# Kernel tuning notes

Measured on AMD Instinct MI355X. Metric: run time of the kernel, lower is better.

Reference implementation:

```python
import jax, jax.numpy as jnp
import numpy as np

B, C, N = 2, 6, 2048      # batch, channels (xyz+3 extra), points per cloud
K, NS = 64, 32            # top-k keypoints, ball-query group size
D = 32                    # deep feature dim (num_feat)
RADIUS = 1.0              # ball query radius (sample_and_group)
VR, VS = 1.0, 0.4         # voxelize range / step -> 6^3 = 216 candidates


def setup_inputs() -> dict:
    key = jax.random.key(0)
    ks = jax.random.split(key, 16)
    rn = lambda k, s, sc=1.0: jax.random.normal(k, s, dtype=jnp.float32) * sc
    Q, _ = jnp.linalg.qr(jax.random.normal(ks[2], (3, 3), dtype=jnp.float32))
    return {
        "src_pts": rn(ks[0], (B, C, N)),
        "tgt_pts": rn(ks[1], (B, C, N)),
        "R_init": Q,
        "t_init": rn(ks[3], (1, 3), 0.1),
        "W1": rn(ks[4], (C, 64), 0.2), "b1": jnp.zeros((64,), jnp.float32),
        "W2": rn(ks[5], (64, D), 0.2), "b2": jnp.zeros((D,), jnp.float32),
        "Wwl": rn(ks[6], (D, 1), 0.2), "bwl": jnp.zeros((1,), jnp.float32),
        "W3": rn(ks[7], (3 + D, 64), 0.2), "b3": jnp.zeros((64,), jnp.float32),
        "W4": rn(ks[8], (64, D), 0.2), "b4": jnp.zeros((D,), jnp.float32),
    }


def _fe(pts, W1, b1, W2, b2):
    # feat_extraction_layer: shared point-wise MLP. pts [B,C,N] -> xyz [B,N,3], feat [B,N,D]
    x = jnp.transpose(pts, (0, 2, 1))
    xyz = x[..., :3]
    f = jax.nn.relu(x @ W1 + b1)
    f = jax.nn.relu(f @ W2 + b2)
    return xyz, f


def _index_points(pts, idx):
    # pts [B,N,D], idx [B,K,S] -> [B,K,S,D]
    b = pts.shape[0]
    return pts[jnp.arange(b)[:, None, None], idx]


def _sqdist(a, b):
    # a [B,M,3], b [B,N,3] -> [B,M,N]
    return (jnp.sum(a * a, -1)[:, :, None] + jnp.sum(b * b, -1)[:, None, :]
            - 2.0 * jnp.einsum('bmd,bnd->bmn', a, b))


def reference(src_pts, tgt_pts, R_init, t_init, W1, b1, W2, b2, Wwl, bwl, W3, b3, W4, b4):
    b = src_pts.shape[0]
    # FE1 on source
    src_xyz, src_feat = _fe(src_pts, W1, b1, W2, b2)
    # weighting_layer: per-point saliency -> top-K keypoint indices
    w = (src_feat @ Wwl + bwl)[..., 0]                    # [B,N]
    _, kidx = jax.lax.top_k(w, K)                          # [B,K]
    src_T = jnp.transpose(src_pts, (0, 2, 1))              # [B,N,C]
    src_keypts = jnp.take_along_axis(src_T, kidx[:, :, None], axis=1)  # [B,K,C]
    centers = src_keypts[..., :3]
    # sample_and_group: ball query NS nearest-within-radius around each keypoint
    d2 = _sqdist(centers, src_xyz)                         # [B,K,N]
    negd, nn = jax.lax.top_k(-d2, NS)
    group_idx = jnp.where(-negd <= RADIUS ** 2, nn, nn[:, :, :1])
    grouped_xyz = _index_points(src_xyz, group_idx)        # [B,K,NS,3]
    keyfeats = _index_points(src_feat, group_idx)          # [B,K,NS,D]
    src_cat = jnp.concatenate([grouped_xyz - centers[:, :, None, :], keyfeats], -1)
    # FE1 on target
    tgt_xyz, tgt_feat = _fe(tgt_pts, W1, b1, W2, b2)
    # transform keypoints with initial pose, voxelize into candidate grid
    xform = jnp.einsum('ij,bkj->bki', R_init, centers) + t_init
    g = jnp.arange(int(2 * VR / VS) + 1, dtype=jnp.float32) * VS - VR   # 6 steps
    gx, gy, gz = jnp.meshgrid(g, g, g, indexing='ij')
    offs = jnp.stack([gx.ravel(), gy.ravel(), gz.ravel()], -1)          # [216,3]
    cand = xform[:, :, None, :] + offs                      # [B,K,216,3]
    nc = offs.shape[0]
    cand_flat = cand.reshape(b, K * nc, 3)
    # nearest target point per candidate -> gathered deep feature + relative offset
    d2t = _sqdist(cand_flat, tgt_xyz)                       # [B,K*216,N] (dominant buffer)
    nnt = jnp.argmin(d2t, axis=-1)                          # [B,K*216]
    nn_xyz = jnp.take_along_axis(tgt_xyz, nnt[:, :, None], axis=1)
    nn_feat = jnp.take_along_axis(tgt_feat, nnt[:, :, None], axis=1)
    rel = (nn_xyz - cand_flat).reshape(b, K, nc, 3)
    tgt_cat = jnp.concatenate([rel, nn_feat.reshape(b, K, nc, D)], -1)
    # DFE: shared MLP; src branch max-pools over the NS group
    dfe = lambda x: jax.nn.relu(jax.nn.relu(x @ W3 + b3) @ W4 + b4)
    src_dfe = jnp.max(dfe(src_cat), axis=2)                 # [B,K,D]
    tgt_dfe = dfe(tgt_cat)                                  # [B,K,216,D]
    # cpg: similarity -> softmax over candidates -> weighted centroid
    sim = jnp.einsum('bkd,bkcd->bkc', src_dfe, tgt_dfe)
    attn = jax.nn.softmax(sim, axis=-1)
    vcp = jnp.einsum('bkc,bkcd->bkd', attn, cand)           # [B,K,3]
    return src_keypts, vcp
```

## Files before the change

### kernel.cpp

```cpp
#include <hip/hip_runtime.h>
#include <math.h>

#define BB_ 2
#define CC_ 6
#define NN_ 2048
#define KK_ 64
#define NS_ 32
#define DD_ 32
#define NC_ 216
#define HH_ 64

#define OFF_SRC_PACK 0
#define OFF_TGT_PACK 16384
#define OFF_SRC_FEAT 32768
#define OFF_TGT_FEAT 163840
#define OFF_W        294912
#define OFF_CENTERS  299008
#define OFF_XFORM    299392
#define OFF_SRCDFE   299776
#define OFF_NNT      303872

__device__ __forceinline__ unsigned sortable_f32(float f) {
    unsigned u = __float_as_uint(f);
    return (u & 0x80000000u) ? ~u : (u | 0x80000000u);
}
__device__ __forceinline__ float unsortable_f32(unsigned s) {
    unsigned u = (s & 0x80000000u) ? (s ^ 0x80000000u) : ~s;
    return __uint_as_float(u);
}

__device__ __forceinline__ unsigned long long wave_sort64_asc(unsigned long long key, int lane) {
#pragma unroll
    for (int k = 2; k <= 64; k <<= 1) {
#pragma unroll
        for (int j = k >> 1; j > 0; j >>= 1) {
            unsigned long long other = __shfl_xor(key, j);
            bool lower = (lane & j) == 0;
            bool asc = (lane & k) == 0;
            bool takemin = (lower == asc);
            unsigned long long mn = key < other ? key : other;
            unsigned long long mx = key < other ? other : key;
            key = takemin ? mn : mx;
        }
    }
    return key;
}

__device__ __forceinline__ unsigned long long merge_keep_min64(unsigned long long a, unsigned long long b, int lane) {
    unsigned long long br = __shfl(b, 63 - lane);
    unsigned long long m = a < br ? a : br;
#pragma unroll
    for (int j = 32; j > 0; j >>= 1) {
        unsigned long long other = __shfl_xor(m, j);
        bool lower = (lane & j) == 0;
        unsigned long long mn = m < other ? m : other;
        unsigned long long mx = m < other ? other : m;
        m = lower ? mn : mx;
    }
    return m;
}

__device__ __forceinline__ void block_select64_16w(unsigned long long kA, unsigned long long kB,
                                                   unsigned long long* runs, int tid) {
    int w = tid >> 6, lane = tid & 63;
    kA = wave_sort64_asc(kA, lane);
    kB = wave_sort64_asc(kB, lane);
    unsigned long long m = merge_keep_min64(kA, kB, lane);
    runs[w * 64 + lane] = m;
    __syncthreads();
#pragma unroll
    for (int lvl = 8; lvl >= 1; lvl >>= 1) {
        unsigned long long r = 0;
        if (w < lvl) {
            unsigned long long a = runs[w * 64 + lane];
            unsigned long long b = runs[(w + lvl) * 64 + lane];
            r = merge_keep_min64(a, b, lane);
        }
        __syncthreads();
        if (w < lvl) runs[w * 64 + lane] = r;
        __syncthreads();
    }
}

__global__ void fe_kernel(const float* __restrict__ src, const float* __restrict__ tgt,
                          const float* __restrict__ W1, const float* __restrict__ b1,
                          const float* __restrict__ W2, const float* __restrict__ b2,
                          const float* __restrict__ Wwl, const float* __restrict__ bwl,
                          float* __restrict__ ws) {
    int tid = blockIdx.x * blockDim.x + threadIdx.x;
    if (tid >= 2 * BB_ * NN_) return;
    int cloud = tid / (BB_ * NN_);
    int r = tid - cloud * BB_ * NN_;
    int b = r / NN_, n = r % NN_;
    const float* pts = cloud ? tgt : src;
    float x[CC_];
#pragma unroll
    for (int c = 0; c < CC_; ++c) x[c] = pts[(b * CC_ + c) * NN_ + n];
    float bb;
    {
#pragma clang fp contract(off)
        bb = (x[0] * x[0] + x[1] * x[1]) + x[2] * x[2];
    }
    float4* pack = (float4*)(ws + (cloud ? OFF_TGT_PACK : OFF_SRC_PACK));
    pack[b * NN_ + n] = make_float4(x[0], x[1], x[2], bb);

    float h[HH_];
#pragma unroll
    for (int t = 0; t < HH_; ++t) {
        float s = b1[t];
#pragma unroll
        for (int c = 0; c < CC_; ++c) s += x[c] * W1[c * HH_ + t];
        h[t] = fmaxf(s, 0.f);
    }
    float* feat = ws + (cloud ? OFF_TGT_FEAT : OFF_SRC_FEAT) + (size_t)(b * NN_ + n) * DD_;
    float wsum = 0.f;
#pragma unroll 4
    for (int d = 0; d < DD_; ++d) {
        float s = b2[d];
#pragma unroll
        for (int t = 0; t < HH_; ++t) s += h[t] * W2[t * DD_ + d];
        s = fmaxf(s, 0.f);
        feat[d] = s;
        wsum += s * Wwl[d];
    }
    if (cloud == 0) (ws + OFF_W)[b * NN_ + n] = wsum + bwl[0];
}

__global__ void topk_kernel(const float* __restrict__ src, const float* __restrict__ R,
                            const float* __restrict__ t, float* __restrict__ ws,
                            float* __restrict__ out) {
    __shared__ unsigned long long runs[16 * 64];
    int b = blockIdx.x;
    int tid = threadIdx.x, w = tid >> 6, lane = tid & 63;
    const float* wv = ws + OFF_W + b * NN_;
    int jA = w * 128 + lane, jB = jA + 64;
    unsigned long long kA = ((unsigned long long)(~sortable_f32(wv[jA])) << 32) | (unsigned)jA;
    unsigned long long kB = ((unsigned long long)(~sortable_f32(wv[jB])) << 32) | (unsigned)jB;
    block_select64_16w(kA, kB, runs, tid);
    if (tid < KK_) {
        int bi = (int)(runs[tid] & 0xFFFFFFFFu);
        float c3[3];
#pragma unroll
        for (int c = 0; c < CC_; ++c) {
            float v = src[(b * CC_ + c) * NN_ + bi];
            out[(b * KK_ + tid) * CC_ + c] = v;
            if (c < 3) c3[c] = v;
        }
        float* cen = ws + OFF_CENTERS + (b * KK_ + tid) * 3;
        cen[0] = c3[0]; cen[1] = c3[1]; cen[2] = c3[2];
        float* xf = ws + OFF_XFORM + (b * KK_ + tid) * 3;
#pragma unroll
        for (int i = 0; i < 3; ++i) {
#pragma clang fp contract(off)
            xf[i] = ((R[i * 3 + 0] * c3[0] + R[i * 3 + 1] * c3[1]) + R[i * 3 + 2] * c3[2]) + t[i];
        }
    }
}

__global__ __launch_bounds__(576) void mid_kernel(const float* __restrict__ W3, const float* __restrict__ b3,
                                                  const float* __restrict__ W4, const float* __restrict__ b4,
                                                  float* __restrict__ ws) {
    __shared__ union U {
        float4 pk[NN_];
        struct {
            unsigned long long runs[8 * 64];
            float hs[NS_][HH_];
            float outs[NS_][DD_];
        } s;
    } u;
    int blk = blockIdx.x;
    int tid = threadIdx.x;
    if (blk < 2 * BB_ * KK_) {
        int bk = blk >> 1;
        int half = blk & 1;
        int b = bk / KK_;
        const float4* pack = (const float4*)(ws + OFF_TGT_PACK) + b * NN_;
        for (int j = tid; j < NN_; j += 576) {
            u.pk[j ^ ((j >> 6) & 7)] = pack[j];
        }
        const float* xf = ws + OFF_XFORM + bk * 3;
        float x0 = xf[0], x1 = xf[1], x2 = xf[2];
        __syncthreads();

        int lg = tid >> 5;
        int chunk = tid & 31;
        int grp = half * 18 + lg;
        int ix = grp / 6, iy = grp % 6;
        float cx = x0 + (ix * 0.4f - 1.0f);
        float cy = x1 + (iy * 0.4f - 1.0f);
        float cxy2;
        {
#pragma clang fp contract(off)
            cxy2 = cx * cx + cy * cy;
        }
        float m2x = -2.0f * cx, m2y = -2.0f * cy;
        float aaz[6], m2z[6];
#pragma unroll
        for (int z = 0; z < 6; ++z) {
            float cz = x2 + (z * 0.4f - 1.0f);
            {
#pragma clang fp contract(off)
                aaz[z] = cxy2 + cz * cz;
            }
            m2z[z] = -2.0f * cz;
        }
        float bv[6];
        int bi[6];
#pragma unroll
        for (int z = 0; z < 6; ++z) { bv[z] = INFINITY; bi[z] = 0; }
        int base = chunk * 64;
        int sw = chunk & 7;
        for (int i = 0; i < 64; ++i) {
            int j = base + i;
            float4 p = u.pk[base + (i ^ sw)];
            float txy;
            {
#pragma clang fp contract(off)
                txy = m2x * p.x + m2y * p.y;
            }
#pragma unroll
            for (int z = 0; z < 6; ++z) {
                float d2;
                {
#pragma clang fp contract(off)
                    d2 = (aaz[z] + p.w) + (txy + m2z[z] * p.z);
                }
                if (d2 < bv[z]) { bv[z] = d2; bi[z] = j; }
            }
        }
        int* nnt = (int*)ws + OFF_NNT + bk * NC_ + grp * 6;
#pragma unroll
        for (int z = 0; z < 6; ++z) {
            unsigned long long key = ((unsigned long long)sortable_f32(bv[z]) << 32) | (unsigned)bi[z];
#pragma unroll
            for (int m = 1; m <= 16; m <<= 1) {
                unsigned long long other = __shfl_xor(key, m);
                key = other < key ? other : key;
            }
            if (chunk == 0) nnt[z] = (int)(key & 0xFFFFFFFFu);
        }
    } else {
        int bk = blk - 2 * BB_ * KK_;
        int b = bk / KK_;
        int w = tid >> 6, lane = tid & 63;
        const float* cen = ws + OFF_CENTERS + bk * 3;
        float c0 = cen[0], c1 = cen[1], c2 = cen[2];
        float aa;
        {
#pragma clang fp contract(off)
            aa = (c0 * c0 + c1 * c1) + c2 * c2;
        }
        float m2x = -2.0f * c0, m2y = -2.0f * c1, m2z = -2.0f * c2;
        const float4* pack = (const float4*)(ws + OFF_SRC_PACK) + b * NN_;
        if (w < 8) {
            unsigned long long k4[4];
#pragma unroll
            for (int q = 0; q < 4; ++q) {
                int j = w * 256 + q * 64 + lane;
                float4 p = pack[j];
                float d2;
                {
#pragma clang fp contract(off)
                    d2 = (aa + p.w) + ((m2x * p.x + m2y * p.y) + m2z * p.z);
                }
                k4[q] = ((unsigned long long)sortable_f32(d2) << 32) | (unsigned)j;
            }
            unsigned long long m1 = merge_keep_min64(wave_sort64_asc(k4[0], lane),
                                                     wave_sort64_asc(k4[1], lane), lane);
            unsigned long long m2 = merge_keep_min64(wave_sort64_asc(k4[2], lane),
                                                     wave_sort64_asc(k4[3], lane), lane);
            u.s.runs[w * 64 + lane] = merge_keep_min64(m1, m2, lane);
        }
        __syncthreads();
#pragma unroll
        for (int lvl = 4; lvl >= 1; lvl >>= 1) {
            unsigned long long r = 0;
            if (w < lvl) {
                r = merge_keep_min64(u.s.runs[w * 64 + lane], u.s.runs[(w + lvl) * 64 + lane], lane);
            }
            __syncthreads();
            if (w < lvl) u.s.runs[w * 64 + lane] = r;
            __syncthreads();
        }
        const float* feats = ws + OFF_SRC_FEAT + (size_t)b * NN_ * DD_;
        unsigned long long key0 = u.s.runs[0];
        if (w < 8) {
#pragma unroll
            for (int ss = 0; ss < 4; ++ss) {
                int s = w * 4 + ss;
                unsigned long long key = u.s.runs[s];
                float dd = unsortable_f32((unsigned)(key >> 32));
                int j = (dd <= 1.0f) ? (int)(key & 0xFFFFFFFFu) : (int)(key0 & 0xFFFFFFFFu);
                float4 p = pack[j];
                float r0 = p.x - c0, r1 = p.y - c1, r2 = p.z - c2;
                const float* f = feats + (size_t)j * DD_;
                float acc = b3[lane] + r0 * W3[0 * HH_ + lane] + r1 * W3[1 * HH_ + lane] + r2 * W3[2 * HH_ + lane];
#pragma unroll 8
                for (int d = 0; d < DD_; ++d) acc += f[d] * W3[(3 + d) * HH_ + lane];
                u.s.hs[s][lane] = fmaxf(acc, 0.f);
            }
        }
        __syncthreads();
        for (int idx = tid; idx < NS_ * DD_; idx += 576) {
            int s2 = idx >> 5, di = idx & 31;
            float o = b4[di];
#pragma unroll 8
            for (int t2 = 0; t2 < HH_; ++t2) o += u.s.hs[s2][t2] * W4[t2 * DD_ + di];
            u.s.outs[s2][di] = fmaxf(o, 0.f);
        }
        __syncthreads();
        if (tid < DD_) {
            float m = -INFINITY;
#pragma unroll 8
            for (int s = 0; s < NS_; ++s) m = fmaxf(m, u.s.outs[s][tid]);
            (ws + OFF_SRCDFE)[bk * DD_ + tid] = m;
        }
    }
}

__global__ void simvcp_kernel(const float* __restrict__ W3, const float* __restrict__ b3,
                              const float* __restrict__ W4, const float* __restrict__ b4,
                              float* __restrict__ ws, float* __restrict__ out) {
    __shared__ float sims[NC_];
    int bk = blockIdx.x;
    int b = bk / KK_;
    int tid = threadIdx.x;
    const float* xf = ws + OFF_XFORM + bk * 3;
    if (tid < NC_) {
        int c = tid;
        int ix = c / 36, iy = (c / 6) % 6, iz = c % 6;
        float cx = xf[0] + (ix * 0.4f - 1.0f);
        float cy = xf[1] + (iy * 0.4f - 1.0f);
        float cz = xf[2] + (iz * 0.4f - 1.0f);
        int bi = ((const int*)ws)[OFF_NNT + bk * NC_ + c];
        float4 p = ((const float4*)(ws + OFF_TGT_PACK))[b * NN_ + bi];
        float x[3 + DD_];
        x[0] = p.x - cx; x[1] = p.y - cy; x[2] = p.z - cz;
        const float* f = ws + OFF_TGT_FEAT + ((size_t)b * NN_ + bi) * DD_;
#pragma unroll
        for (int d = 0; d < DD_; ++d) x[3 + d] = f[d];
        float o[DD_];
#pragma unroll
        for (int d = 0; d < DD_; ++d) o[d] = b4[d];
        for (int t = 0; t < HH_; ++t) {
            float acc = b3[t];
#pragma unroll
            for (int cc = 0; cc < 3 + DD_; ++cc) acc += x[cc] * W3[cc * HH_ + t];
            float ht = fmaxf(acc, 0.f);
#pragma unroll
            for (int d = 0; d < DD_; ++d) o[d] += ht * W4[t * DD_ + d];
        }
        const float* sd = ws + OFF_SRCDFE + bk * DD_;
        float sim = 0.f;
#pragma unroll
        for (int d = 0; d < DD_; ++d) sim += fmaxf(o[d], 0.f) * sd[d];
        sims[c] = sim;
    }
    __syncthreads();
    if (tid < 64) {
        int lane = tid;
        float m = -INFINITY;
        for (int c = lane; c < NC_; c += 64) m = fmaxf(m, sims[c]);
#pragma unroll
        for (int sh = 32; sh; sh >>= 1) m = fmaxf(m, __shfl_xor(m, sh));
        float se = 0.f, v0 = 0.f, v1 = 0.f, v2 = 0.f;
        for (int c = lane; c < NC_; c += 64) {
            float e = expf(sims[c] - m);
            int ix = c / 36, iy = (c / 6) % 6, iz = c % 6;
            se += e;
            v0 += e * (xf[0] + (ix * 0.4f - 1.0f));
            v1 += e * (xf[1] + (iy * 0.4f - 1.0f));
            v2 += e * (xf[2] + (iz * 0.4f - 1.0f));
        }
#pragma unroll
        for (int sh = 32; sh; sh >>= 1) {
            se += __shfl_xor(se, sh);
            v0 += __shfl_xor(v0, sh);
            v1 += __shfl_xor(v1, sh);
            v2 += __shfl_xor(v2, sh);
        }
        if (lane == 0) {
            float inv = 1.0f / se;
            float* oo = out + BB_ * KK_ * CC_ + bk * 3;
            oo[0] = v0 * inv;
            oo[1] = v1 * inv;
            oo[2] = v2 * inv;
        }
    }
}

extern "C" void kernel_launch(void* const* d_in, const int* in_sizes, int n_in,
                              void* d_out, int out_size, void* d_ws, size_t ws_size,
                              hipStream_t stream) {
    const float* src = (const float*)d_in[0];
    const float* tgt = (const float*)d_in[1];
    const float* R   = (const float*)d_in[2];
    const float* t   = (const float*)d_in[3];
    const float* W1  = (const float*)d_in[4];
    const float* b1  = (const float*)d_in[5];
    const float* W2  = (const float*)d_in[6];
    const float* b2  = (const float*)d_in[7];
    const float* Wwl = (const float*)d_in[8];
    const float* bwl = (const float*)d_in[9];
    const float* W3  = (const float*)d_in[10];
    const float* b3  = (const float*)d_in[11];
    const float* W4  = (const float*)d_in[12];
    const float* b4  = (const float*)d_in[13];
    float* ws  = (float*)d_ws;
    float* out = (float*)d_out;

    fe_kernel<<<(2 * BB_ * NN_ + 127) / 128, 128, 0, stream>>>(src, tgt, W1, b1, W2, b2, Wwl, bwl, ws);
    topk_kernel<<<BB_, 1024, 0, stream>>>(src, R, t, ws, out);
    mid_kernel<<<2 * BB_ * KK_ + BB_ * KK_, 576, 0, stream>>>(W3, b3, W4, b4, ws);
    simvcp_kernel<<<BB_ * KK_, 256, 0, stream>>>(W3, b3, W4, b4, ws, out);
}
```

Baseline: 82.53 us.

## Fuse pipeline into single cooperative kernel with grid barrier and recomputed features

Replaces the four launches with one cooperative kernel of 128 blocks, one per keypoint. Each block first computes saliency for a 32-point slice, then waits at an atomic-counter grid barrier. After that every block redundantly runs the top-k selection, the candidate nearest-neighbour search and the source grouping. Target features are recomputed only for the 216 matched neighbours instead of for all target points. This removes launch gaps and global-memory round trips, at the cost of duplicated top-k work per block, a spin barrier, and an extra memset launch.

```diff
diff --git a/kernel.cpp b/kernel.cpp
--- a/kernel.cpp
+++ b/kernel.cpp
@@ -9,16 +9,10 @@
 #define DD_ 32
 #define NC_ 216
 #define HH_ 64
-
-#define OFF_SRC_PACK 0
-#define OFF_TGT_PACK 16384
-#define OFF_SRC_FEAT 32768
-#define OFF_TGT_FEAT 163840
-#define OFF_W        294912
-#define OFF_CENTERS  299008
-#define OFF_XFORM    299392
-#define OFF_SRCDFE   299776
-#define OFF_NNT      303872
+#define NBLK_ 128
+
+#define OFF_W        0
+#define OFF_BAR      4096
 
 __device__ __forceinline__ unsigned sortable_f32(float f) {
     unsigned u = __float_as_uint(f);
@@ -60,331 +54,384 @@
     return m;
 }
 
-__device__ __forceinline__ void block_select64_16w(unsigned long long kA, unsigned long long kB,
-                                                   unsigned long long* runs, int tid) {
-    int w = tid >> 6, lane = tid & 63;
-    kA = wave_sort64_asc(kA, lane);
-    kB = wave_sort64_asc(kB, lane);
-    unsigned long long m = merge_keep_min64(kA, kB, lane);
-    runs[w * 64 + lane] = m;
-    __syncthreads();
-#pragma unroll
-    for (int lvl = 8; lvl >= 1; lvl >>= 1) {
-        unsigned long long r = 0;
-        if (w < lvl) {
-            unsigned long long a = runs[w * 64 + lane];
-            unsigned long long b = runs[(w + lvl) * 64 + lane];
-            r = merge_keep_min64(a, b, lane);
-        }
-        __syncthreads();
-        if (w < lvl) runs[w * 64 + lane] = r;
-        __syncthreads();
-    }
-}
-
-__global__ void fe_kernel(const float* __restrict__ src, const float* __restrict__ tgt,
-                          const float* __restrict__ W1, const float* __restrict__ b1,
-                          const float* __restrict__ W2, const float* __restrict__ b2,
-                          const float* __restrict__ Wwl, const float* __restrict__ bwl,
-                          float* __restrict__ ws) {
-    int tid = blockIdx.x * blockDim.x + threadIdx.x;
-    if (tid >= 2 * BB_ * NN_) return;
-    int cloud = tid / (BB_ * NN_);
-    int r = tid - cloud * BB_ * NN_;
-    int b = r / NN_, n = r % NN_;
-    const float* pts = cloud ? tgt : src;
-    float x[CC_];
-#pragma unroll
-    for (int c = 0; c < CC_; ++c) x[c] = pts[(b * CC_ + c) * NN_ + n];
-    float bb;
-    {
-#pragma clang fp contract(off)
-        bb = (x[0] * x[0] + x[1] * x[1]) + x[2] * x[2];
-    }
-    float4* pack = (float4*)(ws + (cloud ? OFF_TGT_PACK : OFF_SRC_PACK));
-    pack[b * NN_ + n] = make_float4(x[0], x[1], x[2], bb);
-
-    float h[HH_];
-#pragma unroll
-    for (int t = 0; t < HH_; ++t) {
-        float s = b1[t];
-#pragma unroll
-        for (int c = 0; c < CC_; ++c) s += x[c] * W1[c * HH_ + t];
-        h[t] = fmaxf(s, 0.f);
-    }
-    float* feat = ws + (cloud ? OFF_TGT_FEAT : OFF_SRC_FEAT) + (size_t)(b * NN_ + n) * DD_;
-    float wsum = 0.f;
-#pragma unroll 4
-    for (int d = 0; d < DD_; ++d) {
-        float s = b2[d];
-#pragma unroll
-        for (int t = 0; t < HH_; ++t) s += h[t] * W2[t * DD_ + d];
-        s = fmaxf(s, 0.f);
-        feat[d] = s;
-        wsum += s * Wwl[d];
-    }
-    if (cloud == 0) (ws + OFF_W)[b * NN_ + n] = wsum + bwl[0];
-}
-
-__global__ void topk_kernel(const float* __restrict__ src, const float* __restrict__ R,
-                            const float* __restrict__ t, float* __restrict__ ws,
-                            float* __restrict__ out) {
-    __shared__ unsigned long long runs[16 * 64];
-    int b = blockIdx.x;
-    int tid = threadIdx.x, w = tid >> 6, lane = tid & 63;
-    const float* wv = ws + OFF_W + b * NN_;
-    int jA = w * 128 + lane, jB = jA + 64;
-    unsigned long long kA = ((unsigned long long)(~sortable_f32(wv[jA])) << 32) | (unsigned)jA;
-    unsigned long long kB = ((unsigned long long)(~sortable_f32(wv[jB])) << 32) | (unsigned)jB;
-    block_select64_16w(kA, kB, runs, tid);
-    if (tid < KK_) {
-        int bi = (int)(runs[tid] & 0xFFFFFFFFu);
-        float c3[3];
-#pragma unroll
-        for (int c = 0; c < CC_; ++c) {
-            float v = src[(b * CC_ + c) * NN_ + bi];
-            out[(b * KK_ + tid) * CC_ + c] = v;
-            if (c < 3) c3[c] = v;
-        }
-        float* cen = ws + OFF_CENTERS + (b * KK_ + tid) * 3;
-        cen[0] = c3[0]; cen[1] = c3[1]; cen[2] = c3[2];
-        float* xf = ws + OFF_XFORM + (b * KK_ + tid) * 3;
-#pragma unroll
-        for (int i = 0; i < 3; ++i) {
-#pragma clang fp contract(off)
-            xf[i] = ((R[i * 3 + 0] * c3[0] + R[i * 3 + 1] * c3[1]) + R[i * 3 + 2] * c3[2]) + t[i];
-        }
-    }
-}
-
-__global__ __launch_bounds__(576) void mid_kernel(const float* __restrict__ W3, const float* __restrict__ b3,
-                                                  const float* __restrict__ W4, const float* __restrict__ b4,
-                                                  float* __restrict__ ws) {
-    __shared__ union U {
+__global__ __launch_bounds__(576) void mega2_kernel(
+        const float* __restrict__ src, const float* __restrict__ tgt,
+        const float* __restrict__ R, const float* __restrict__ t,
+        const float* __restrict__ W1, const float* __restrict__ b1,
+        const float* __restrict__ W2, const float* __restrict__ b2,
+        const float* __restrict__ Wwl, const float* __restrict__ bwl,
+        const float* __restrict__ W3, const float* __restrict__ b3,
+        const float* __restrict__ W4, const float* __restrict__ b4,
+        float* __restrict__ ws, float* __restrict__ out) {
+    __shared__ union {
+        struct { float fpts[32][CC_]; float h[32][HH_]; float f[32][DD_]; } fe;
+        unsigned long long runs[8 * 64];
         float4 pk[NN_];
         struct {
-            unsigned long long runs[8 * 64];
+            unsigned long long runs2[8 * 64];
+            float spts[NS_][CC_];
             float hs[NS_][HH_];
+            float sfeat[NS_][DD_];
             float outs[NS_][DD_];
-        } s;
+        } sg;
+        struct { float th[108][HH_]; float tfeat[NC_][DD_]; } tf;
     } u;
+    __shared__ float bcast[8];
+    __shared__ int   nnt216[NC_];
+    __shared__ float tall[NC_][CC_];
+    __shared__ int   sidx[NS_];
+    __shared__ float sdfe[DD_];
+    __shared__ float sims[NC_];
+
     int blk = blockIdx.x;
     int tid = threadIdx.x;
-    if (blk < 2 * BB_ * KK_) {
-        int bk = blk >> 1;
-        int half = blk & 1;
-        int b = bk / KK_;
-        const float4* pack = (const float4*)(ws + OFF_TGT_PACK) + b * NN_;
-        for (int j = tid; j < NN_; j += 576) {
-            u.pk[j ^ ((j >> 6) & 7)] = pack[j];
-        }
-        const float* xf = ws + OFF_XFORM + bk * 3;
-        float x0 = xf[0], x1 = xf[1], x2 = xf[2];
-        __syncthreads();
-
-        int lg = tid >> 5;
-        int chunk = tid & 31;
-        int grp = half * 18 + lg;
-        int ix = grp / 6, iy = grp % 6;
-        float cx = x0 + (ix * 0.4f - 1.0f);
-        float cy = x1 + (iy * 0.4f - 1.0f);
-        float cxy2;
-        {
-#pragma clang fp contract(off)
-            cxy2 = cx * cx + cy * cy;
-        }
-        float m2x = -2.0f * cx, m2y = -2.0f * cy;
-        float aaz[6], m2z[6];
-#pragma unroll
-        for (int z = 0; z < 6; ++z) {
-            float cz = x2 + (z * 0.4f - 1.0f);
-            {
-#pragma clang fp contract(off)
-                aaz[z] = cxy2 + cz * cz;
-            }
-            m2z[z] = -2.0f * cz;
-        }
-        float bv[6];
-        int bi[6];
-#pragma unroll
-        for (int z = 0; z < 6; ++z) { bv[z] = INFINITY; bi[z] = 0; }
-        int base = chunk * 64;
-        int sw = chunk & 7;
-        for (int i = 0; i < 64; ++i) {
-            int j = base + i;
-            float4 p = u.pk[base + (i ^ sw)];
-            float txy;
-            {
-#pragma clang fp contract(off)
-                txy = m2x * p.x + m2y * p.y;
-            }
-#pragma unroll
-            for (int z = 0; z < 6; ++z) {
-                float d2;
-                {
-#pragma clang fp contract(off)
-                    d2 = (aaz[z] + p.w) + (txy + m2z[z] * p.z);
-                }
-                if (d2 < bv[z]) { bv[z] = d2; bi[z] = j; }
-            }
-        }
-        int* nnt = (int*)ws + OFF_NNT + bk * NC_ + grp * 6;
-#pragma unroll
-        for (int z = 0; z < 6; ++z) {
-            unsigned long long key = ((unsigned long long)sortable_f32(bv[z]) << 32) | (unsigned)bi[z];
-#pragma unroll
-            for (int m = 1; m <= 16; m <<= 1) {
-                unsigned long long other = __shfl_xor(key, m);
-                key = other < key ? other : key;
-            }
-            if (chunk == 0) nnt[z] = (int)(key & 0xFFFFFFFFu);
-        }
-    } else {
-        int bk = blk - 2 * BB_ * KK_;
-        int b = bk / KK_;
-        int w = tid >> 6, lane = tid & 63;
-        const float* cen = ws + OFF_CENTERS + bk * 3;
-        float c0 = cen[0], c1 = cen[1], c2 = cen[2];
-        float aa;
-        {
-#pragma clang fp contract(off)
-            aa = (c0 * c0 + c1 * c1) + c2 * c2;
-        }
-        float m2x = -2.0f * c0, m2y = -2.0f * c1, m2z = -2.0f * c2;
-        const float4* pack = (const float4*)(ws + OFF_SRC_PACK) + b * NN_;
+    int w = tid >> 6, lane = tid & 63;
+    int bk = blk;
+    int bat = bk / KK_;
+    int kth = bk % KK_;
+    float* wbuf = ws + OFF_W;
+    unsigned* ctr = (unsigned*)(ws + OFF_BAR);
+
+    {
+        int p0 = blk * 32;
+        for (int idx = tid; idx < 32 * CC_; idx += 576) {
+            int pt = idx / CC_, c = idx % CC_;
+            int g = p0 + pt; int bb = g / NN_, n = g % NN_;
+            u.fe.fpts[pt][c] = src[(bb * CC_ + c) * NN_ + n];
+        }
+        __syncthreads();
+        for (int idx = tid; idx < 32 * HH_; idx += 576) {
+            int pt = idx >> 6, tt = idx & 63;
+            float s = b1[tt];
+#pragma unroll
+            for (int c = 0; c < CC_; ++c) s += u.fe.fpts[pt][c] * W1[c * HH_ + tt];
+            u.fe.h[pt][tt] = fmaxf(s, 0.f);
+        }
+        __syncthreads();
+        for (int idx = tid; idx < 32 * DD_; idx += 576) {
+            int pt = idx >> 5, d = idx & 31;
+            float s = b2[d];
+#pragma unroll 8
+            for (int tt = 0; tt < HH_; ++tt) s += u.fe.h[pt][tt] * W2[tt * DD_ + d];
+            u.fe.f[pt][d] = fmaxf(s, 0.f);
+        }
+        __syncthreads();
+        if (tid < 32) {
+            float wsum = 0.f;
+#pragma unroll 8
+            for (int d = 0; d < DD_; ++d) wsum += u.fe.f[tid][d] * Wwl[d];
+            wsum += bwl[0];
+            __hip_atomic_store(&wbuf[p0 + tid], wsum, __ATOMIC_RELAXED, __HIP_MEMORY_SCOPE_AGENT);
+        }
+        __syncthreads();
+        if (tid == 0)
+            __hip_atomic_fetch_add(ctr, 1u, __ATOMIC_RELEASE, __HIP_MEMORY_SCOPE_AGENT);
+        if (tid == 0) {
+            while (__hip_atomic_load(ctr, __ATOMIC_RELAXED, __HIP_MEMORY_SCOPE_AGENT) < (unsigned)NBLK_)
+                __builtin_amdgcn_s_sleep(4);
+        }
+        __syncthreads();
+    }
+
+    {
         if (w < 8) {
             unsigned long long k4[4];
 #pragma unroll
             for (int q = 0; q < 4; ++q) {
                 int j = w * 256 + q * 64 + lane;
-                float4 p = pack[j];
-                float d2;
-                {
-#pragma clang fp contract(off)
-                    d2 = (aa + p.w) + ((m2x * p.x + m2y * p.y) + m2z * p.z);
-                }
-                k4[q] = ((unsigned long long)sortable_f32(d2) << 32) | (unsigned)j;
+                float wv = __hip_atomic_load(&wbuf[bat * NN_ + j], __ATOMIC_RELAXED, __HIP_MEMORY_SCOPE_AGENT);
+                k4[q] = ((unsigned long long)(~sortable_f32(wv)) << 32) | (unsigned)j;
             }
             unsigned long long m1 = merge_keep_min64(wave_sort64_asc(k4[0], lane),
                                                      wave_sort64_asc(k4[1], lane), lane);
             unsigned long long m2 = merge_keep_min64(wave_sort64_asc(k4[2], lane),
                                                      wave_sort64_asc(k4[3], lane), lane);
-            u.s.runs[w * 64 + lane] = merge_keep_min64(m1, m2, lane);
+            u.runs[w * 64 + lane] = merge_keep_min64(m1, m2, lane);
         }
         __syncthreads();
 #pragma unroll
         for (int lvl = 4; lvl >= 1; lvl >>= 1) {
             unsigned long long r = 0;
-            if (w < lvl) {
-                r = merge_keep_min64(u.s.runs[w * 64 + lane], u.s.runs[(w + lvl) * 64 + lane], lane);
-            }
-            __syncthreads();
-            if (w < lvl) u.s.runs[w * 64 + lane] = r;
-            __syncthreads();
-        }
-        const float* feats = ws + OFF_SRC_FEAT + (size_t)b * NN_ * DD_;
-        unsigned long long key0 = u.s.runs[0];
+            if (w < lvl) r = merge_keep_min64(u.runs[w * 64 + lane], u.runs[(w + lvl) * 64 + lane], lane);
+            __syncthreads();
+            if (w < lvl) u.runs[w * 64 + lane] = r;
+            __syncthreads();
+        }
+        if (tid == 0) {
+            int bi = (int)(u.runs[kth] & 0xFFFFFFFFu);
+            float c3[3];
+#pragma unroll
+            for (int c = 0; c < CC_; ++c) {
+                float v = src[(bat * CC_ + c) * NN_ + bi];
+                out[bk * CC_ + c] = v;
+                if (c < 3) c3[c] = v;
+            }
+            bcast[0] = c3[0]; bcast[1] = c3[1]; bcast[2] = c3[2];
+#pragma unroll
+            for (int i = 0; i < 3; ++i) {
+#pragma clang fp contract(off)
+                bcast[3 + i] = ((R[i * 3 + 0] * c3[0] + R[i * 3 + 1] * c3[1]) + R[i * 3 + 2] * c3[2]) + t[i];
+            }
+        }
+        __syncthreads();
+    }
+
+    {
+        for (int j = tid; j < NN_; j += 576) {
+            float px = tgt[(bat * CC_ + 0) * NN_ + j];
+            float py = tgt[(bat * CC_ + 1) * NN_ + j];
+            float pz = tgt[(bat * CC_ + 2) * NN_ + j];
+            float pw;
+            {
+#pragma clang fp contract(off)
+                pw = (px * px + py * py) + pz * pz;
+            }
+            u.pk[j ^ ((j >> 6) & 7)] = make_float4(px, py, pz, pw);
+        }
+        __syncthreads();
+        float x0 = bcast[3], x1 = bcast[4], x2 = bcast[5];
+        int lg = tid >> 5;
+        int chunk = tid & 31;
+        int base = chunk * 64;
+        int sw = chunk & 7;
+        for (int pass = 0; pass < 2; ++pass) {
+            int grp = pass * 18 + lg;
+            int ix = grp / 6, iy = grp % 6;
+            float cx = x0 + (ix * 0.4f - 1.0f);
+            float cy = x1 + (iy * 0.4f - 1.0f);
+            float cxy2;
+            {
+#pragma clang fp contract(off)
+                cxy2 = cx * cx + cy * cy;
+            }
+            float m2x = -2.0f * cx, m2y = -2.0f * cy;
+            float aaz[6], m2z[6];
+#pragma unroll
+            for (int z = 0; z < 6; ++z) {
+                float cz = x2 + (z * 0.4f - 1.0f);
+                {
+#pragma clang fp contract(off)
+                    aaz[z] = cxy2 + cz * cz;
+                }
+                m2z[z] = -2.0f * cz;
+            }
+            float bv[6];
+            int bi[6];
+#pragma unroll
+            for (int z = 0; z < 6; ++z) { bv[z] = INFINITY; bi[z] = 0; }
+            for (int i = 0; i < 64; ++i) {
+                int j = base + i;
+                float4 p = u.pk[base + (i ^ sw)];
+                float txy;
+                {
+#pragma clang fp contract(off)
+                    txy = m2x * p.x + m2y * p.y;
+                }
+#pragma unroll
+                for (int z = 0; z < 6; ++z) {
+                    float d2;
+                    {
+#pragma clang fp contract(off)
+                        d2 = (aaz[z] + p.w) + (txy + m2z[z] * p.z);
+                    }
+                    if (d2 < bv[z]) { bv[z] = d2; bi[z] = j; }
+                }
+            }
+#pragma unroll
+            for (int z = 0; z < 6; ++z) {
+                unsigned long long key = ((unsigned long long)sortable_f32(bv[z]) << 32) | (unsigned)bi[z];
+#pragma unroll
+                for (int m = 1; m <= 16; m <<= 1) {
+                    unsigned long long other = __shfl_xor(key, m);
+                    key = other < key ? other : key;
+                }
+                if (chunk == 0) nnt216[grp * 6 + z] = (int)(key & 0xFFFFFFFFu);
+            }
+        }
+        __syncthreads();
+    }
+
+    {
+        float c0 = bcast[0], c1 = bcast[1], c2 = bcast[2];
+        float aa;
+        {
+#pragma clang fp contract(off)
+            aa = (c0 * c0 + c1 * c1) + c2 * c2;
+        }
+        float m2x = -2.0f * c0, m2y = -2.0f * c1, m2z = -2.0f * c2;
+        if (w < 8) {
+            unsigned long long k4[4];
+#pragma unroll
+            for (int q = 0; q < 4; ++q) {
+                int j = w * 256 + q * 64 + lane;
+                float px = src[(bat * CC_ + 0) * NN_ + j];
+                float py = src[(bat * CC_ + 1) * NN_ + j];
+                float pz = src[(bat * CC_ + 2) * NN_ + j];
+                float d2;
+                {
+#pragma clang fp contract(off)
+                    float pw = (px * px + py * py) + pz * pz;
+                    d2 = (aa + pw) + ((m2x * px + m2y * py) + m2z * pz);
+                }
+                k4[q] = ((unsigned long long)sortable_f32(d2) << 32) | (unsigned)j;
+            }
+            unsigned long long m1 = merge_keep_min64(wave_sort64_asc(k4[0], lane),
+                                                     wave_sort64_asc(k4[1], lane), lane);
+            unsigned long long m2 = merge_keep_min64(wave_sort64_asc(k4[2], lane),
+                                                     wave_sort64_asc(k4[3], lane), lane);
+            u.sg.runs2[w * 64 + lane] = merge_keep_min64(m1, m2, lane);
+        }
+        __syncthreads();
+#pragma unroll
+        for (int lvl = 4; lvl >= 1; lvl >>= 1) {
+            unsigned long long r = 0;
+            if (w < lvl) r = merge_keep_min64(u.sg.runs2[w * 64 + lane], u.sg.runs2[(w + lvl) * 64 + lane], lane);
+            __syncthreads();
+            if (w < lvl) u.sg.runs2[w * 64 + lane] = r;
+            __syncthreads();
+        }
+        if (tid < NS_) {
+            unsigned long long key = u.sg.runs2[tid];
+            unsigned long long key0 = u.sg.runs2[0];
+            float dd = unsortable_f32((unsigned)(key >> 32));
+            sidx[tid] = (dd <= 1.0f) ? (int)(key & 0xFFFFFFFFu) : (int)(key0 & 0xFFFFFFFFu);
+        }
+        __syncthreads();
+        for (int idx = tid; idx < NS_ * CC_; idx += 576) {
+            int pt = idx / CC_, c = idx % CC_;
+            u.sg.spts[pt][c] = src[(bat * CC_ + c) * NN_ + sidx[pt]];
+        }
+        __syncthreads();
+        for (int idx = tid; idx < NS_ * HH_; idx += 576) {
+            int pt = idx >> 6, tt = idx & 63;
+            float s = b1[tt];
+#pragma unroll
+            for (int c = 0; c < CC_; ++c) s += u.sg.spts[pt][c] * W1[c * HH_ + tt];
+            u.sg.hs[pt][tt] = fmaxf(s, 0.f);
+        }
+        __syncthreads();
+        for (int idx = tid; idx < NS_ * DD_; idx += 576) {
+            int pt = idx >> 5, d = idx & 31;
+            float s = b2[d];
+#pragma unroll 8
+            for (int tt = 0; tt < HH_; ++tt) s += u.sg.hs[pt][tt] * W2[tt * DD_ + d];
+            u.sg.sfeat[pt][d] = fmaxf(s, 0.f);
+        }
+        __syncthreads();
         if (w < 8) {
 #pragma unroll
             for (int ss = 0; ss < 4; ++ss) {
                 int s = w * 4 + ss;
-                unsigned long long key = u.s.runs[s];
-                float dd = unsortable_f32((unsigned)(key >> 32));
-                int j = (dd <= 1.0f) ? (int)(key & 0xFFFFFFFFu) : (int)(key0 & 0xFFFFFFFFu);
-                float4 p = pack[j];
-                float r0 = p.x - c0, r1 = p.y - c1, r2 = p.z - c2;
-                const float* f = feats + (size_t)j * DD_;
+                float r0 = u.sg.spts[s][0] - c0, r1 = u.sg.spts[s][1] - c1, r2 = u.sg.spts[s][2] - c2;
                 float acc = b3[lane] + r0 * W3[0 * HH_ + lane] + r1 * W3[1 * HH_ + lane] + r2 * W3[2 * HH_ + lane];
 #pragma unroll 8
-                for (int d = 0; d < DD_; ++d) acc += f[d] * W3[(3 + d) * HH_ + lane];
-                u.s.hs[s][lane] = fmaxf(acc, 0.f);
+                for (int d = 0; d < DD_; ++d) acc += u.sg.sfeat[s][d] * W3[(3 + d) * HH_ + lane];
+                u.sg.hs[s][lane] = fmaxf(acc, 0.f);
             }
         }
         __syncthreads();
         for (int idx = tid; idx < NS_ * DD_; idx += 576) {
-            int s2 = idx >> 5, di = idx & 31;
-            float o = b4[di];
-#pragma unroll 8
-            for (int t2 = 0; t2 < HH_; ++t2) o += u.s.hs[s2][t2] * W4[t2 * DD_ + di];
-            u.s.outs[s2][di] = fmaxf(o, 0.f);
+            int s = idx >> 5, d = idx & 31;
+            float o = b4[d];
+#pragma unroll 8
+            for (int tt = 0; tt < HH_; ++tt) o += u.sg.hs[s][tt] * W4[tt * DD_ + d];
+            u.sg.outs[s][d] = fmaxf(o, 0.f);
         }
         __syncthreads();
         if (tid < DD_) {
             float m = -INFINITY;
 #pragma unroll 8
-            for (int s = 0; s < NS_; ++s) m = fmaxf(m, u.s.outs[s][tid]);
-            (ws + OFF_SRCDFE)[bk * DD_ + tid] = m;
-        }
-    }
-}
-
-__global__ void simvcp_kernel(const float* __restrict__ W3, const float* __restrict__ b3,
-                              const float* __restrict__ W4, const float* __restrict__ b4,
-                              float* __restrict__ ws, float* __restrict__ out) {
-    __shared__ float sims[NC_];
-    int bk = blockIdx.x;
-    int b = bk / KK_;
-    int tid = threadIdx.x;
-    const float* xf = ws + OFF_XFORM + bk * 3;
-    if (tid < NC_) {
-        int c = tid;
-        int ix = c / 36, iy = (c / 6) % 6, iz = c % 6;
-        float cx = xf[0] + (ix * 0.4f - 1.0f);
-        float cy = xf[1] + (iy * 0.4f - 1.0f);
-        float cz = xf[2] + (iz * 0.4f - 1.0f);
-        int bi = ((const int*)ws)[OFF_NNT + bk * NC_ + c];
-        float4 p = ((const float4*)(ws + OFF_TGT_PACK))[b * NN_ + bi];
-        float x[3 + DD_];
-        x[0] = p.x - cx; x[1] = p.y - cy; x[2] = p.z - cz;
-        const float* f = ws + OFF_TGT_FEAT + ((size_t)b * NN_ + bi) * DD_;
-#pragma unroll
-        for (int d = 0; d < DD_; ++d) x[3 + d] = f[d];
-        float o[DD_];
-#pragma unroll
-        for (int d = 0; d < DD_; ++d) o[d] = b4[d];
-        for (int t = 0; t < HH_; ++t) {
-            float acc = b3[t];
-#pragma unroll
-            for (int cc = 0; cc < 3 + DD_; ++cc) acc += x[cc] * W3[cc * HH_ + t];
-            float ht = fmaxf(acc, 0.f);
-#pragma unroll
-            for (int d = 0; d < DD_; ++d) o[d] += ht * W4[t * DD_ + d];
-        }
-        const float* sd = ws + OFF_SRCDFE + bk * DD_;
-        float sim = 0.f;
-#pragma unroll
-        for (int d = 0; d < DD_; ++d) sim += fmaxf(o[d], 0.f) * sd[d];
-        sims[c] = sim;
-    }
-    __syncthreads();
-    if (tid < 64) {
-        int lane = tid;
-        float m = -INFINITY;
-        for (int c = lane; c < NC_; c += 64) m = fmaxf(m, sims[c]);
-#pragma unroll
-        for (int sh = 32; sh; sh >>= 1) m = fmaxf(m, __shfl_xor(m, sh));
-        float se = 0.f, v0 = 0.f, v1 = 0.f, v2 = 0.f;
-        for (int c = lane; c < NC_; c += 64) {
-            float e = expf(sims[c] - m);
+            for (int s = 0; s < NS_; ++s) m = fmaxf(m, u.sg.outs[s][tid]);
+            sdfe[tid] = m;
+        }
+        __syncthreads();
+    }
+
+    {
+        for (int idx = tid; idx < NC_ * CC_; idx += 576) {
+            int pt = idx / CC_, c = idx % CC_;
+            tall[pt][c] = tgt[(bat * CC_ + c) * NN_ + nnt216[pt]];
+        }
+        __syncthreads();
+        for (int ch = 0; ch < 2; ++ch) {
+            for (int idx = tid; idx < 108 * HH_; idx += 576) {
+                int pl = idx >> 6, tt = idx & 63;
+                int pt = ch * 108 + pl;
+                float s = b1[tt];
+#pragma unroll
+                for (int c = 0; c < CC_; ++c) s += tall[pt][c] * W1[c * HH_ + tt];
+                u.tf.th[pl][tt] = fmaxf(s, 0.f);
+            }
+            __syncthreads();
+            for (int idx = tid; idx < 108 * DD_; idx += 576) {
+                int pl = idx >> 5, d = idx & 31;
+                int pt = ch * 108 + pl;
+                float s = b2[d];
+#pragma unroll 8
+                for (int tt = 0; tt < HH_; ++tt) s += u.tf.th[pl][tt] * W2[tt * DD_ + d];
+                u.tf.tfeat[pt][d] = fmaxf(s, 0.f);
+            }
+            __syncthreads();
+        }
+    }
+
+    {
+        float x0 = bcast[3], x1 = bcast[4], x2 = bcast[5];
+        if (tid < NC_) {
+            int c = tid;
             int ix = c / 36, iy = (c / 6) % 6, iz = c % 6;
-            se += e;
-            v0 += e * (xf[0] + (ix * 0.4f - 1.0f));
-            v1 += e * (xf[1] + (iy * 0.4f - 1.0f));
-            v2 += e * (xf[2] + (iz * 0.4f - 1.0f));
-        }
-#pragma unroll
-        for (int sh = 32; sh; sh >>= 1) {
-            se += __shfl_xor(se, sh);
-            v0 += __shfl_xor(v0, sh);
-            v1 += __shfl_xor(v1, sh);
-            v2 += __shfl_xor(v2, sh);
-        }
-        if (lane == 0) {
-            float inv = 1.0f / se;
-            float* oo = out + BB_ * KK_ * CC_ + bk * 3;
-            oo[0] = v0 * inv;
-            oo[1] = v1 * inv;
-            oo[2] = v2 * inv;
+            float cx = x0 + (ix * 0.4f - 1.0f);
+            float cy = x1 + (iy * 0.4f - 1.0f);
+            float cz = x2 + (iz * 0.4f - 1.0f);
+            float x[3 + DD_];
+            x[0] = tall[c][0] - cx; x[1] = tall[c][1] - cy; x[2] = tall[c][2] - cz;
+#pragma unroll
+            for (int d = 0; d < DD_; ++d) x[3 + d] = u.tf.tfeat[c][d];
+            float o[DD_];
+#pragma unroll
+            for (int d = 0; d < DD_; ++d) o[d] = b4[d];
+            for (int tt = 0; tt < HH_; ++tt) {
+                float acc = b3[tt];
+#pragma unroll
+                for (int cc = 0; cc < 3 + DD_; ++cc) acc += x[cc] * W3[cc * HH_ + tt];
+                float ht = fmaxf(acc, 0.f);
+#pragma unroll
+                for (int d = 0; d < DD_; ++d) o[d] += ht * W4[tt * DD_ + d];
+            }
+            float sim = 0.f;
+#pragma unroll
+            for (int d = 0; d < DD_; ++d) sim += fmaxf(o[d], 0.f) * sdfe[d];
+            sims[c] = sim;
+        }
+        __syncthreads();
+        if (tid < 64) {
+            float m = -INFINITY;
+            for (int c = lane; c < NC_; c += 64) m = fmaxf(m, sims[c]);
+#pragma unroll
+            for (int sh = 32; sh; sh >>= 1) m = fmaxf(m, __shfl_xor(m, sh));
+            float se = 0.f, v0 = 0.f, v1 = 0.f, v2 = 0.f;
+            for (int c = lane; c < NC_; c += 64) {
+                float e = expf(sims[c] - m);
+                int ix = c / 36, iy = (c / 6) % 6, iz = c % 6;
+                se += e;
+                v0 += e * (x0 + (ix * 0.4f - 1.0f));
+                v1 += e * (x1 + (iy * 0.4f - 1.0f));
+                v2 += e * (x2 + (iz * 0.4f - 1.0f));
+            }
+#pragma unroll
+            for (int sh = 32; sh; sh >>= 1) {
+                se += __shfl_xor(se, sh);
+                v0 += __shfl_xor(v0, sh);
+                v1 += __shfl_xor(v1, sh);
+                v2 += __shfl_xor(v2, sh);
+            }
+            if (lane == 0) {
+                float inv = 1.0f / se;
+                float* oo = out + BB_ * KK_ * CC_ + bk * 3;
+                oo[0] = v0 * inv;
+                oo[1] = v1 * inv;
+                oo[2] = v2 * inv;
+            }
         }
     }
 }
@@ -409,8 +456,17 @@
     float* ws  = (float*)d_ws;
     float* out = (float*)d_out;
 
-    fe_kernel<<<(2 * BB_ * NN_ + 127) / 128, 128, 0, stream>>>(src, tgt, W1, b1, W2, b2, Wwl, bwl, ws);
-    topk_kernel<<<BB_, 1024, 0, stream>>>(src, R, t, ws, out);
-    mid_kernel<<<2 * BB_ * KK_ + BB_ * KK_, 576, 0, stream>>>(W3, b3, W4, b4, ws);
-    simvcp_kernel<<<BB_ * KK_, 256, 0, stream>>>(W3, b3, W4, b4, ws, out);
-}
+    hipMemsetAsync(ws + OFF_BAR, 0, sizeof(unsigned), stream);
+
+    void* args[] = {(void*)&src, (void*)&tgt, (void*)&R, (void*)&t,
+                    (void*)&W1, (void*)&b1, (void*)&W2, (void*)&b2,
+                    (void*)&Wwl, (void*)&bwl, (void*)&W3, (void*)&b3,
+                    (void*)&W4, (void*)&b4, (void*)&ws, (void*)&out};
+    hipError_t e = hipLaunchCooperativeKernel((const void*)mega2_kernel,
+                                              dim3(NBLK_), dim3(576),
+                                              args, 0, stream);
+    if (e != hipSuccess) {
+        mega2_kernel<<<NBLK_, 576, 0, stream>>>(src, tgt, R, t, W1, b1, W2, b2,
+                                                Wwl, bwl, W3, b3, W4, b4, ws, out);
+    }
+}
```

Measured after the change: 138.0 us. 67.2% more time.
